# Optimization experiments

Hardware: AMD Instinct MI355X
Metric: run time of the kernel (lower is better)

The kernel has to match this reference:

```python
import jax, jax.numpy as jnp
import numpy as np

K = 98          # fixed_n_tokens
HEADS = 8
EPS = 1e-5      # BatchNorm eps


def setup_inputs() -> dict:
    key = jax.random.key(0)
    ks = jax.random.split(key, 8)
    B, C, H, W = 32, 384, 56, 56

    def p(k, shape, scale=0.02):
        return jax.random.normal(k, shape, jnp.float32) * scale

    return {
        "x": jax.random.normal(ks[0], (B, C, H, W), jnp.float32),
        "qkv_w": p(ks[1], (3 * C, C)),
        "qkv_b": jnp.zeros((3 * C,), jnp.float32),
        "proj_w": p(ks[2], (C, C)),
        "proj_b": jnp.zeros((C,), jnp.float32),
        "bn_g": jnp.ones((C,), jnp.float32),
        "bn_b": jnp.zeros((C,), jnp.float32),
        "fc1_w": p(ks[3], (C, C)),
        "fc1_b": jnp.zeros((C,), jnp.float32),
        "fc2_w": p(ks[4], (C, C)),
        "fc2_b": jnp.zeros((C,), jnp.float32),
        "dw_w": p(ks[5], (C, 1, 3, 3), 0.1),  # depthwise 3x3, groups=C
        "dw_b": jnp.zeros((C,), jnp.float32),
    }


def reference(x, qkv_w, qkv_b, proj_w, proj_b, bn_g, bn_b,
              fc1_w, fc1_b, fc2_w, fc2_b, dw_w, dw_b):
    B, C, H, W = x.shape
    N = H * W
    head_dim = C // HEADS
    scale = head_dim ** -0.5

    # ---- salience top-k selection (pool_size=(1,1): no pooling) ----
    xf = x.reshape(B, C, N)
    scores = jnp.sum(xf * xf, axis=1)                       # [B, N]
    _, top_idx = jax.lax.top_k(scores, K)                   # [B, K]
    top = jnp.take_along_axis(xf, top_idx[:, None, :], axis=2)   # [B, C, K]
    bg = (xf.sum(2) - top.sum(2)) / (N - K)                 # [B, C]
    tokens = jnp.concatenate([top, bg[:, :, None]], axis=2)      # [B, C, K+1]
    tokens = tokens.transpose(0, 2, 1)                      # [B, K+1, C]

    # ---- tiny attention over K+1 tokens ----
    n = K + 1
    qkv = tokens @ qkv_w.T + qkv_b                          # [B, n, 3C]
    qkv = qkv.reshape(B, n, 3, HEADS, head_dim).transpose(2, 0, 3, 1, 4)
    q, k, v = qkv[0], qkv[1], qkv[2]                        # [B, h, n, d]
    attn = jax.nn.softmax(scale * jnp.einsum('bhnd,bhmd->bhnm', q, k), axis=-1)
    res = jnp.einsum('bhnm,bhmd->bhnd', attn, v)            # [B, h, n, d]
    attn_out = res.transpose(0, 1, 3, 2).reshape(B, C, n)   # b (h d) n

    # ---- scatter-restore: bg token everywhere, top tokens at their slots ----
    top_res, bg_res = attn_out[:, :, :K], attn_out[:, :, K:]    # [B,C,K], [B,C,1]
    restored = jnp.broadcast_to(bg_res, (B, C, N))
    bi = jnp.arange(B)[:, None, None]
    ci = jnp.arange(C)[None, :, None]
    restored = restored.at[bi, ci, top_idx[:, None, :]].set(top_res)
    restored = restored.reshape(B, C, H, W)  # interpolate is identity (same size)

    # ---- conv branch: BN (batch stats) -> fc1 -> gelu -> dwconv -> fc2 ----
    mu = x.mean(axis=(0, 2, 3), keepdims=True)
    var = x.var(axis=(0, 2, 3), keepdims=True)
    xn = (x - mu) * jax.lax.rsqrt(var + EPS)
    xn = xn * bn_g[None, :, None, None] + bn_b[None, :, None, None]
    h1 = jnp.einsum('bchw,oc->bohw', xn, fc1_w) + fc1_b[None, :, None, None]
    h1 = jax.nn.gelu(h1, approximate=False)
    h2 = jax.lax.conv_general_dilated(
        h1, dw_w, window_strides=(1, 1), padding='SAME',
        dimension_numbers=('NCHW', 'OIHW', 'NCHW'), feature_group_count=C)
    h2 = h2 + dw_b[None, :, None, None]
    conv_out = jnp.einsum('bchw,oc->bohw', h2, fc2_w) + fc2_b[None, :, None, None]

    combined = restored + conv_out
    return jnp.einsum('bchw,oc->bohw', combined, proj_w) + proj_b[None, :, None, None]
```

## Files before the change

kernel.cpp:

```cpp
#include <hip/hip_runtime.h>
#include <hip/hip_bf16.h>
#include <math.h>

typedef unsigned short u16;
typedef short short8 __attribute__((ext_vector_type(8)));
typedef float floatx4 __attribute__((ext_vector_type(4)));

#define B_    32
#define C_    384
#define N_    3136
#define K_TOP 98
#define NTOK  99
#define TOKS  (B_ * NTOK)
#define HEADS_ 8
#define HD    48
#define KDIM  384

__device__ __forceinline__ float b2f(u16 u) {
    unsigned int x = ((unsigned int)u) << 16;
    return __builtin_bit_cast(float, x);
}
__device__ __forceinline__ u16 f2b(float f) {
    unsigned int x = __builtin_bit_cast(unsigned int, f);
    unsigned int r = (x + 0x7fffu + ((x >> 16) & 1u)) >> 16;
    return (u16)r;
}
__device__ __forceinline__ u16 tob16(float f) { return f2b(f); }
__device__ __forceinline__ u16 tob16(u16 u) { return u; }


__global__ void k_zero(float* sumsq) { sumsq[threadIdx.x] = 0.f; }

__global__ void k_cvt(const float* __restrict__ src, u16* __restrict__ dst, int n) {
    int i = blockIdx.x * 256 + threadIdx.x;
    if (i < n) dst[i] = f2b(src[i]);
}

__global__ void k_scores(const float* __restrict__ x, float* __restrict__ scores) {
    int gid = blockIdx.x * 256 + threadIdx.x;
    int b = gid / N_;
    int p = gid - b * N_;
    const float* xp = x + (size_t)b * C_ * N_ + p;
    float s = 0.f;
#pragma unroll 8
    for (int c = 0; c < C_; ++c) {
        float v = xp[(size_t)c * N_];
        s += v * v;
    }
    scores[gid] = s;
}

__global__ void k_chsum(const float* __restrict__ x, float* __restrict__ ch_sum,
                        float* __restrict__ sumsq) {
    int bc = blockIdx.x;
    int c = bc % C_;
    const float* xp = x + (size_t)bc * N_;
    float s1 = 0.f, s2 = 0.f;
    for (int p = threadIdx.x; p < N_; p += 256) {
        float v = xp[p];
        s1 += v; s2 += v * v;
    }
#pragma unroll
    for (int off = 32; off; off >>= 1) {
        s1 += __shfl_down(s1, off);
        s2 += __shfl_down(s2, off);
    }
    __shared__ float r1[4], r2[4];
    int wave = threadIdx.x >> 6;
    if ((threadIdx.x & 63) == 0) { r1[wave] = s1; r2[wave] = s2; }
    __syncthreads();
    if (threadIdx.x == 0) {
        float a = r1[0] + r1[1] + r1[2] + r1[3];
        float b2 = r2[0] + r2[1] + r2[2] + r2[3];
        ch_sum[bc] = a;
        atomicAdd(&sumsq[c], b2);
    }
}

__launch_bounds__(1024)
__global__ void k_topk(const float* __restrict__ scores, int* __restrict__ idx,
                       int* __restrict__ istop) {
    int b = blockIdx.x;
    int tid = threadIdx.x;
    __shared__ unsigned int keys[N_];
    __shared__ int hist[4096];
    __shared__ unsigned int sh_prefix;
    __shared__ int sh_g;
    __shared__ int c1, tc;
    __shared__ int idxbuf[K_TOP];
    __shared__ int tiebuf[128];

    for (int p = tid; p < N_; p += 1024) {
        keys[p] = __builtin_bit_cast(unsigned int, scores[b * N_ + p]);
        istop[b * N_ + p] = 0;
    }

    int Kcur = K_TOP;
    unsigned int prefix = 0;
    int m = 0;
#pragma unroll
    for (int pass = 0; pass < 3; ++pass) {
        const int shift = (pass == 0) ? 20 : (pass == 1 ? 8 : 0);
        const int nbins = (pass == 2) ? 256 : 4096;
        const unsigned int pm = (pass == 0) ? 0u : (pass == 1 ? 0xFFF00000u : 0xFFFFFF00u);
        for (int i = tid; i < nbins; i += 1024) hist[i] = 0;
        __syncthreads();
        for (int p = tid; p < N_; p += 1024) {
            unsigned int u = keys[p];
            if ((u & pm) == prefix) atomicAdd(&hist[(u >> shift) & (nbins - 1)], 1);
        }
        __syncthreads();
        if (tid < 64) {
            int lane = tid;
            int nch = nbins >> 6;
            int s = 0;
            for (int j = 0; j < nch; ++j) s += hist[lane * nch + j];
            int suf = s;
#pragma unroll
            for (int off = 1; off < 64; off <<= 1) {
                int v = __shfl_down(suf, off);
                if (lane + off < 64) suf += v;
            }
            int above = suf - s;
            if (suf >= Kcur && above < Kcur) {
                int acc = above;
                int bin = (lane + 1) * nch - 1;
                for (;; --bin) {
                    int h = hist[bin];
                    if (acc + h >= Kcur) break;
                    acc += h;
                }
                sh_prefix = prefix | ((unsigned int)bin << shift);
                sh_g = acc;
            }
        }
        __syncthreads();
        prefix = sh_prefix;
        m += sh_g;
        Kcur -= sh_g;
    }

    unsigned int lo = prefix;
    if (tid == 0) { c1 = 0; tc = 0; }
    __syncthreads();
    for (int p = tid; p < N_; p += 1024) {
        unsigned int u = keys[p];
        if (u > lo) { int pos = atomicAdd(&c1, 1); idxbuf[pos] = p; }
        else if (u == lo) { int pos = atomicAdd(&tc, 1); if (pos < 128) tiebuf[pos] = p; }
    }
    __syncthreads();
    if (tid == 0) {
        int need = K_TOP - m;
        if (tc <= 128) {
            int cnt = tc;
            for (int r = 0; r < need; ++r) {
                int mi = r;
                for (int q = r + 1; q < cnt; ++q) if (tiebuf[q] < tiebuf[mi]) mi = q;
                int t = tiebuf[mi]; tiebuf[mi] = tiebuf[r]; tiebuf[r] = t;
                idxbuf[m + r] = t;
            }
        } else {
            int picked = 0;
            for (int p = 0; p < N_ && picked < need; ++p)
                if (keys[p] == lo) { idxbuf[m + picked] = p; ++picked; }
        }
    }
    __syncthreads();
    if (tid < K_TOP) {
        int ib = idxbuf[tid];
        idx[b * K_TOP + tid] = ib;
        istop[b * N_ + ib] = tid + 1;
    }
}

__launch_bounds__(256)
__global__ void k_tokens(const float* __restrict__ x, const int* __restrict__ idx,
                         const float* __restrict__ ch_sum, u16* __restrict__ tokensT) {
    int b = blockIdx.x, cg = blockIdx.y;
    __shared__ int il[K_TOP];
    int tid = threadIdx.x;
    if (tid < K_TOP) il[tid] = idx[b * K_TOP + tid];
    __syncthreads();
    int cl = tid >> 2;
    int js = tid & 3;
    int c = cg * 64 + cl;
    const float* xp = x + (size_t)b * C_ * N_ + (size_t)c * N_;
    u16* tp = tokensT + (size_t)c * TOKS + b * NTOK;
    float s = 0.f;
    for (int j = js; j < K_TOP; j += 4) {
        float v = xp[il[j]];
        tp[j] = f2b(v);
        s += v;
    }
    s += __shfl_down(s, 2);
    s += __shfl_down(s, 1);
    if (js == 0) {
        float bg = (ch_sum[b * C_ + c] - s) * (1.0f / (float)(N_ - K_TOP));
        tp[K_TOP] = f2b(bg);
    }
}

__global__ void k_bnfin(const float* ch_sum, const float* sumsq, const float* bn_g,
                        const float* bn_b, float* a_scale, float* b_shift) {
    int c = threadIdx.x;
    float s = 0.f;
    for (int b = 0; b < B_; ++b) s += ch_sum[b * C_ + c];
    float inv_n = 1.0f / (float)(B_ * N_);
    float mu = s * inv_n;
    float var = sumsq[c] * inv_n - mu * mu;
    float a = rsqrtf(var + 1e-5f) * bn_g[c];
    a_scale[c] = a;
    b_shift[c] = bn_b[c] - mu * a;
}

__global__ void k_bias2p(const float* __restrict__ fc2_w, const float* __restrict__ fc2_b,
                         const float* __restrict__ dw_b, float* __restrict__ bias2p) {
    int c = blockIdx.x * 4 + (threadIdx.x >> 6);
    int l = threadIdx.x & 63;
    float acc = 0.f;
    for (int k = l; k < C_; k += 64) acc += fc2_w[c * C_ + k] * dw_b[k];
#pragma unroll
    for (int off = 32; off; off >>= 1) acc += __shfl_down(acc, off);
    if (l == 0) bias2p[c] = acc + fc2_b[c];
}

__global__ void k_biasM(const float* __restrict__ proj_w, const float* __restrict__ proj_b,
                        const float* __restrict__ bias2p, float* __restrict__ biasM) {
    int o = blockIdx.x * 4 + (threadIdx.x >> 6);
    int l = threadIdx.x & 63;
    float acc = 0.f;
    for (int c = l; c < C_; c += 64) acc += proj_w[o * C_ + c] * bias2p[c];
#pragma unroll
    for (int off = 32; off; off >>= 1) acc += __shfl_down(acc, off);
    if (l == 0) biasM[o] = acc + proj_b[o];
}

__global__ void k_bias1(const float* __restrict__ fc1_w, const float* __restrict__ fc1_b,
                        const float* __restrict__ b_shift, float* __restrict__ bias1) {
    int o = blockIdx.x * 4 + (threadIdx.x >> 6);
    int l = threadIdx.x & 63;
    float acc = 0.f;
    for (int c = l; c < C_; c += 64) acc += fc1_w[o * C_ + c] * b_shift[c];
#pragma unroll
    for (int off = 32; off; off >>= 1) acc += __shfl_down(acc, off);
    if (l == 0) bias1[o] = acc + fc1_b[o];
}

__global__ void k_cbias(const float* __restrict__ proj_w, const float* __restrict__ biasM,
                        const float* __restrict__ bgres, float* __restrict__ cbias) {
    int b = blockIdx.y;
    int o = blockIdx.x * 4 + (threadIdx.x >> 6);
    int l = threadIdx.x & 63;
    float acc = 0.f;
    for (int c = l; c < C_; c += 64) acc += proj_w[o * C_ + c] * bgres[b * C_ + c];
#pragma unroll
    for (int off = 32; off; off >>= 1) acc += __shfl_down(acc, off);
    if (l == 0) cbias[b * C_ + o] = acc + biasM[o];
}

__global__ void k_mw(const float* __restrict__ proj_w, const float* __restrict__ fc2_w,
                     u16* __restrict__ Mw) {
    int o = blockIdx.x, c = threadIdx.x;
    float acc = 0.f;
    for (int k = 0; k < C_; ++k) acc += proj_w[o * C_ + k] * fc2_w[k * C_ + c];
    Mw[o * C_ + c] = f2b(acc);
}

__global__ void k_w1p(const float* fc1_w, const float* a_scale, u16* W1p) {
    int i = blockIdx.x * 256 + threadIdx.x;
    if (i < C_ * C_) {
        int c = i % C_;
        W1p[i] = f2b(fc1_w[i] * a_scale[c]);
    }
}

__launch_bounds__(256)
__global__ void k_gemm_qkv(const u16* __restrict__ A, const u16* __restrict__ Bsrc,
                           const float* __restrict__ biasB, float* __restrict__ outF) {
    const int ldB = TOKS, NC = TOKS;
    int m0 = blockIdx.x * 128;
    int n0 = blockIdx.y * 64;
    int tid = threadIdx.x;
    int lane = tid & 63;
    int wave = tid >> 6;
    int wm0 = (wave >> 1) * 64;
    int wn0 = (wave & 1) * 32;
    int lm = lane & 15;
    int quad = lane >> 4;

    __shared__ __attribute__((aligned(16))) u16 Al[128 * 32];
    __shared__ __attribute__((aligned(16))) u16 Bl[64 * 32];

    floatx4 acc[4][2];
#pragma unroll
    for (int i = 0; i < 4; ++i)
#pragma unroll
        for (int j = 0; j < 2; ++j)
#pragma unroll
            for (int r = 0; r < 4; ++r) acc[i][j][r] = 0.f;

    int ar = tid >> 2;
    int akc = (tid & 3) * 8;
    int bp = tid & 63;
    int bgi = tid >> 6;
    int bswz = ((bgi ^ ((bp >> 1) & 3)) & 3) * 8;
    int bcol = n0 + bp;
    bool bok = bcol < NC;

    for (int kt = 0; kt < 12; ++kt) {
        int k0 = kt * 32;
        __syncthreads();
#pragma unroll
        for (int i = 0; i < 2; ++i) {
            int r = ar + i * 64;
            short8 v = *(const short8*)(const void*)(A + (size_t)(m0 + r) * KDIM + k0 + akc);
            *(short8*)(void*)&Al[r * 32 + akc] = v;
        }
        {
            const u16* src = Bsrc + (size_t)(k0 + bgi * 8) * ldB + bcol;
            short8 v;
#pragma unroll
            for (int j = 0; j < 8; ++j)
                v[j] = bok ? (short)src[(size_t)j * ldB] : (short)0;
            *(short8*)(void*)&Bl[bp * 32 + bswz] = v;
        }
        __syncthreads();
        short8 af[4], bfv[2];
#pragma unroll
        for (int mt = 0; mt < 4; ++mt)
            af[mt] = *(const short8*)(const void*)&Al[(wm0 + mt * 16 + lm) * 32 + quad * 8];
#pragma unroll
        for (int nt = 0; nt < 2; ++nt) {
            int prow = wn0 + nt * 16 + lm;
            int sw = ((quad ^ ((prow >> 1) & 3)) & 3) * 8;
            bfv[nt] = *(const short8*)(const void*)&Bl[prow * 32 + sw];
        }
#pragma unroll
        for (int mt = 0; mt < 4; ++mt)
#pragma unroll
            for (int nt = 0; nt < 2; ++nt)
                acc[mt][nt] = __builtin_amdgcn_mfma_f32_16x16x32_bf16(af[mt], bfv[nt], acc[mt][nt], 0, 0, 0);
    }

#pragma unroll
    for (int nt = 0; nt < 2; ++nt) {
        int col = n0 + wn0 + nt * 16 + lm;
        if (col >= NC) continue;
#pragma unroll
        for (int mt = 0; mt < 4; ++mt)
#pragma unroll
            for (int r = 0; r < 4; ++r) {
                int o = m0 + wm0 + mt * 16 + quad * 4 + r;
                outF[(size_t)o * TOKS + col] = acc[mt][nt][r] + biasB[o];
            }
    }
}

template<int MODE, typename TB>
__launch_bounds__(512, 4)
__global__ void k_gemm2(const u16* __restrict__ A, const TB* __restrict__ B0, long bStride,
                        const float* __restrict__ biasF,
                        float* __restrict__ outF,
                        u16* __restrict__ outB,
                        const float* __restrict__ cbias, const int* __restrict__ istop,
                        const float* __restrict__ delta2) {
    const int ldB = N_;
    int b = blockIdx.y;
    int n0 = blockIdx.x * 64;
    const TB* Bsrc = B0 + (size_t)b * bStride;
    int tid = threadIdx.x;
    int lane = tid & 63;
    int wave = tid >> 6;
    int wm0 = wave * 48;
    int lm = lane & 15;
    int quad = lane >> 4;

    __shared__ __attribute__((aligned(16))) u16 Bl[2][64 * 128];

    int sc = tid & 63;
    int kg = tid >> 6;
    int w0 = ((kg ^ (sc & 7)) * 8);
    const TB* bsp = Bsrc + (size_t)n0 + sc;

    floatx4 acc[3][4];
#pragma unroll
    for (int i = 0; i < 3; ++i)
#pragma unroll
        for (int j = 0; j < 4; ++j)
#pragma unroll
            for (int r = 0; r < 4; ++r) acc[i][j][r] = 0.f;

    TB rv0[8], rv1[8];
    {
        const TB* p0 = bsp + (size_t)(kg * 8) * ldB;
        const TB* p1 = bsp + (size_t)(64 + kg * 8) * ldB;
#pragma unroll
        for (int j = 0; j < 8; ++j) { rv0[j] = p0[(size_t)j * ldB]; rv1[j] = p1[(size_t)j * ldB]; }
        short8 s0, s1;
#pragma unroll
        for (int j = 0; j < 8; ++j) { s0[j] = (short)tob16(rv0[j]); s1[j] = (short)tob16(rv1[j]); }
        *(short8*)(void*)&Bl[0][sc * 128 + w0] = s0;
        *(short8*)(void*)&Bl[0][sc * 128 + 64 + w0] = s1;
    }
    __syncthreads();

    for (int ch = 0; ch < 3; ++ch) {
        int cur = ch & 1;
        if (ch < 2) {
            const TB* p0 = bsp + (size_t)((ch + 1) * 128 + kg * 8) * ldB;
            const TB* p1 = bsp + (size_t)((ch + 1) * 128 + 64 + kg * 8) * ldB;
#pragma unroll
            for (int j = 0; j < 8; ++j) { rv0[j] = p0[(size_t)j * ldB]; rv1[j] = p1[(size_t)j * ldB]; }
        }
#pragma unroll
        for (int kt = 0; kt < 4; ++kt) {
            int k0 = ch * 128 + kt * 32;
            short8 af[3], bfv[4];
#pragma unroll
            for (int mt = 0; mt < 3; ++mt)
                af[mt] = *(const short8*)(const void*)(A + (size_t)(wm0 + mt * 16 + lm) * KDIM + k0 + quad * 8);
#pragma unroll
            for (int nt = 0; nt < 4; ++nt) {
                int pc = nt * 16 + lm;
                int win = kt * 4 + quad;
                bfv[nt] = *(const short8*)(const void*)&Bl[cur][pc * 128 + ((win ^ (pc & 7)) * 8)];
            }
#pragma unroll
            for (int mt = 0; mt < 3; ++mt)
#pragma unroll
                for (int nt = 0; nt < 4; ++nt)
                    acc[mt][nt] = __builtin_amdgcn_mfma_f32_16x16x32_bf16(af[mt], bfv[nt], acc[mt][nt], 0, 0, 0);
        }
        if (ch < 2) {
            short8 s0, s1;
#pragma unroll
            for (int j = 0; j < 8; ++j) { s0[j] = (short)tob16(rv0[j]); s1[j] = (short)tob16(rv1[j]); }
            *(short8*)(void*)&Bl[cur ^ 1][sc * 128 + w0] = s0;
            *(short8*)(void*)&Bl[cur ^ 1][sc * 128 + 64 + w0] = s1;
            __syncthreads();
        }
    }

#pragma unroll
    for (int nt = 0; nt < 4; ++nt) {
        int ocol = n0 + nt * 16 + lm;
        int tt = 0;
        if (MODE == 3) tt = istop[b * N_ + ocol];
#pragma unroll
        for (int mt = 0; mt < 3; ++mt) {
#pragma unroll
            for (int r = 0; r < 4; ++r) {
                int o = wm0 + mt * 16 + quad * 4 + r;
                float val = acc[mt][nt][r];
                if (MODE == 2) {
                    outF[(size_t)o * N_ + ocol] = val;
                } else if (MODE == 1) {
                    val += biasF[o];
                    float g = 0.5f * val * (1.0f + erff(val * 0.70710678118654752f));
                    outB[(size_t)b * C_ * N_ + (size_t)o * N_ + ocol] = f2b(g);
                } else {
                    val += cbias[b * C_ + o];
                    if (tt) val += delta2[(size_t)o * N_ + b * K_TOP + (tt - 1)];
                    outF[(size_t)b * C_ * N_ + (size_t)o * N_ + ocol] = val;
                }
            }
        }
    }
}


__global__ void k_attn_scores(const float* __restrict__ qkv, float* __restrict__ Sws) {
    int b = blockIdx.x, h = blockIdx.y;
    __shared__ float ql[NTOK * HD], kl[NTOK * HD];
    int tid = threadIdx.x;
    const float scale = 0.14433756729740643f;
    for (int u = tid; u < NTOK * HD; u += 256) {
        int d = u / NTOK, j = u - d * NTOK;
        size_t base = (size_t)(h * HD + d) * TOKS + b * NTOK + j;
        ql[j * HD + d] = qkv[base] * scale;
        kl[j * HD + d] = qkv[base + (size_t)C_ * TOKS];
    }
    __syncthreads();
    float* Sp = Sws + (size_t)(b * HEADS_ + h) * (NTOK * NTOK);
    for (int u = tid; u < NTOK * NTOK; u += 256) {
        int i = u / NTOK, j = u - i * NTOK;
        float s = 0.f;
#pragma unroll 8
        for (int d = 0; d < HD; ++d) s += ql[i * HD + d] * kl[j * HD + d];
        Sp[u] = s;
    }
}

__global__ void k_attn_out(const float* __restrict__ qkv, const float* __restrict__ Sws,
                           u16* __restrict__ diffT, float* __restrict__ bgres) {
    int b = blockIdx.x, h = blockIdx.y;
    __shared__ float vl[NTOK * HD];
    __shared__ float P[NTOK * 100];
    __shared__ float bgrow[HD];
    int tid = threadIdx.x;
    for (int u = tid; u < NTOK * HD; u += 256) {
        int d = u / NTOK, j = u - d * NTOK;
        vl[j * HD + d] = qkv[(size_t)(2 * C_ + h * HD + d) * TOKS + b * NTOK + j];
    }
    __syncthreads();
    const float* Sp = Sws + (size_t)(b * HEADS_ + h) * (NTOK * NTOK);
    if (tid < NTOK) {
        int i = tid;
        float mx = -1e30f;
        for (int j = 0; j < NTOK; ++j) mx = fmaxf(mx, Sp[i * NTOK + j]);
        float sum = 0.f;
        for (int j = 0; j < NTOK; ++j) { float e = expf(Sp[i * NTOK + j] - mx); P[i * 100 + j] = e; sum += e; }
        float inv = 1.f / sum;
        for (int j = 0; j < NTOK; ++j) P[i * 100 + j] *= inv;
    }
    __syncthreads();
    if (tid < HD) {
        int d = tid;
        float a = 0.f;
        for (int j = 0; j < NTOK; ++j) a += P[K_TOP * 100 + j] * vl[j * HD + d];
        bgrow[d] = a;
        bgres[b * C_ + h * HD + d] = a;
    }
    __syncthreads();
    for (int u = tid; u < K_TOP * HD; u += 256) {
        int d = u / K_TOP, i = u - d * K_TOP;
        float a = 0.f;
        for (int j = 0; j < NTOK; ++j) a += P[i * 100 + j] * vl[j * HD + d];
        diffT[(size_t)(h * HD + d) * N_ + b * K_TOP + i] = f2b(a - bgrow[d]);
    }
}

__launch_bounds__(256)
__global__ void k_dwconv(u16* __restrict__ h1, const float* __restrict__ dw_w) {
    int bc = blockIdx.x;
    int c = bc % C_;
    __shared__ __attribute__((aligned(16))) u16 tile[4256];
    int tid = threadIdx.x;
#pragma unroll
    for (int i = tid; i < 532; i += 256)
        *(short8*)(void*)&tile[i * 8] = (short8)0;
    float w[9];
#pragma unroll
    for (int t = 0; t < 9; ++t) w[t] = dw_w[c * 9 + t];
    __syncthreads();
    u16* src = h1 + (size_t)bc * N_;
    for (int i = tid; i < 392; i += 256) {
        int y = i / 7, xg = i - y * 7;
        short8 v = *(const short8*)(const void*)(src + i * 8);
        *(short8*)(void*)&tile[(y + 2) * 72 + xg * 8] = v;
    }
    __syncthreads();
    for (int g = tid; g < 392; g += 256) {
        int y = g / 7, xg = (g - y * 7) * 8;
        float out[8];
#pragma unroll
        for (int t = 0; t < 8; ++t) out[t] = 0.f;
#pragma unroll
        for (int ky = 0; ky < 3; ++ky) {
            const u16* rp = &tile[(y + ky + 1) * 72 + xg];
            short8 mid = *(const short8*)(const void*)rp;
            float r[10];
            r[0] = b2f(rp[-1]);
#pragma unroll
            for (int t = 0; t < 8; ++t) r[t + 1] = b2f((u16)mid[t]);
            r[9] = b2f(rp[8]);
#pragma unroll
            for (int kx = 0; kx < 3; ++kx) {
                float wv = w[ky * 3 + kx];
#pragma unroll
                for (int t = 0; t < 8; ++t) out[t] += wv * r[t + kx];
            }
        }
        short8 o;
#pragma unroll
        for (int t = 0; t < 8; ++t) o[t] = (short)f2b(out[t]);
        *(short8*)(void*)(src + g * 8) = o;
    }
}


extern "C" void kernel_launch(void* const* d_in, const int* in_sizes, int n_in,
                              void* d_out, int out_size, void* d_ws, size_t ws_size,
                              hipStream_t stream) {
    (void)in_sizes; (void)n_in; (void)out_size; (void)ws_size;
    const float* x      = (const float*)d_in[0];
    const float* qkv_w  = (const float*)d_in[1];
    const float* qkv_b  = (const float*)d_in[2];
    const float* proj_w = (const float*)d_in[3];
    const float* proj_b = (const float*)d_in[4];
    const float* bn_g   = (const float*)d_in[5];
    const float* bn_b   = (const float*)d_in[6];
    const float* fc1_w  = (const float*)d_in[7];
    const float* fc1_b  = (const float*)d_in[8];
    const float* fc2_w  = (const float*)d_in[9];
    const float* fc2_b  = (const float*)d_in[10];
    const float* dw_w   = (const float*)d_in[11];
    const float* dw_b   = (const float*)d_in[12];
    float* out = (float*)d_out;

    float* qkvF = (float*)d_out;
    float* Sws  = (float*)((char*)d_out + (size_t)3 * C_ * TOKS * 4);

    char* w = (char*)d_ws;
    constexpr size_t o_h1      = 0;
    constexpr size_t o_scores  = o_h1      + (size_t)B_ * C_ * N_ * 2;
    constexpr size_t o_chsum   = o_scores  + (size_t)B_ * N_ * 4;
    constexpr size_t o_sumsq   = o_chsum   + (size_t)B_ * C_ * 4;
    constexpr size_t o_idx     = o_sumsq   + (size_t)C_ * 4;
    constexpr size_t o_istop   = o_idx     + (size_t)B_ * K_TOP * 4;
    constexpr size_t o_tokens  = o_istop   + (size_t)B_ * N_ * 4;
    constexpr size_t o_ascale  = o_tokens  + (size_t)C_ * TOKS * 2;
    constexpr size_t o_bshift  = o_ascale  + (size_t)C_ * 4;
    constexpr size_t o_w1p     = o_bshift  + (size_t)C_ * 4;
    constexpr size_t o_bias1   = o_w1p     + (size_t)C_ * C_ * 2;
    constexpr size_t o_mw      = o_bias1   + (size_t)C_ * 4;
    constexpr size_t o_biasM   = o_mw      + (size_t)C_ * C_ * 2;
    constexpr size_t o_bias2p  = o_biasM   + (size_t)C_ * 4;
    constexpr size_t o_cbias   = o_bias2p  + (size_t)C_ * 4;
    constexpr size_t o_bgres   = o_cbias   + (size_t)B_ * C_ * 4;
    constexpr size_t o_difft   = o_bgres   + (size_t)B_ * C_ * 4;
    constexpr size_t o_delta2  = o_difft   + (size_t)C_ * N_ * 2;
    constexpr size_t o_wq16    = o_delta2  + (size_t)C_ * N_ * 4;
    constexpr size_t o_pw16    = o_wq16    + (size_t)3 * C_ * C_ * 2;

    u16*   h1      = (u16*)(w + o_h1);
    float* scores  = (float*)(w + o_scores);
    float* ch_sum  = (float*)(w + o_chsum);
    float* sumsq   = (float*)(w + o_sumsq);
    int*   idx     = (int*)(w + o_idx);
    int*   istop   = (int*)(w + o_istop);
    u16*   tokensT = (u16*)(w + o_tokens);
    float* a_scale = (float*)(w + o_ascale);
    float* b_shift = (float*)(w + o_bshift);
    u16*   W1p     = (u16*)(w + o_w1p);
    float* bias1   = (float*)(w + o_bias1);
    u16*   Mw      = (u16*)(w + o_mw);
    float* biasM   = (float*)(w + o_biasM);
    float* bias2p  = (float*)(w + o_bias2p);
    float* cbias   = (float*)(w + o_cbias);
    float* bgres   = (float*)(w + o_bgres);
    u16*   diffT   = (u16*)(w + o_difft);
    float* Delta2  = (float*)(w + o_delta2);
    u16*   Wq16    = (u16*)(w + o_wq16);
    u16*   Pw16    = (u16*)(w + o_pw16);

    k_zero<<<1, C_, 0, stream>>>(sumsq);
    k_scores<<<(B_ * N_) / 256, 256, 0, stream>>>(x, scores);
    k_chsum<<<B_ * C_, 256, 0, stream>>>(x, ch_sum, sumsq);
    k_topk<<<B_, 1024, 0, stream>>>(scores, idx, istop);
    k_tokens<<<dim3(B_, 6), 256, 0, stream>>>(x, idx, ch_sum, tokensT);
    k_bnfin<<<1, C_, 0, stream>>>(ch_sum, sumsq, bn_g, bn_b, a_scale, b_shift);
    k_bias2p<<<96, 256, 0, stream>>>(fc2_w, fc2_b, dw_b, bias2p);
    k_mw<<<C_, C_, 0, stream>>>(proj_w, fc2_w, Mw);
    k_biasM<<<96, 256, 0, stream>>>(proj_w, proj_b, bias2p, biasM);
    k_w1p<<<(C_ * C_ + 255) / 256, 256, 0, stream>>>(fc1_w, a_scale, W1p);
    k_bias1<<<96, 256, 0, stream>>>(fc1_w, fc1_b, b_shift, bias1);
    k_cvt<<<(3 * C_ * C_ + 255) / 256, 256, 0, stream>>>(qkv_w, Wq16, 3 * C_ * C_);
    k_cvt<<<(C_ * C_ + 255) / 256, 256, 0, stream>>>(proj_w, Pw16, C_ * C_);

    k_gemm_qkv<<<dim3(9, 50), 256, 0, stream>>>(Wq16, tokensT, qkv_b, qkvF);
    k_attn_scores<<<dim3(B_, HEADS_), 256, 0, stream>>>(qkvF, Sws);
    k_attn_out<<<dim3(B_, HEADS_), 256, 0, stream>>>(qkvF, Sws, diffT, bgres);
    k_cbias<<<dim3(96, B_), 256, 0, stream>>>(proj_w, biasM, bgres, cbias);
    k_gemm2<2, u16><<<dim3(49, 1), 512, 0, stream>>>(Pw16, diffT, 0,
        nullptr, Delta2, nullptr, nullptr, nullptr, nullptr);
    k_gemm2<1, float><<<dim3(49, 32), 512, 0, stream>>>(W1p, x, (long)C_ * N_,
        bias1, nullptr, h1, nullptr, nullptr, nullptr);
    k_dwconv<<<B_ * C_, 256, 0, stream>>>(h1, dw_w);
    k_gemm2<3, u16><<<dim3(49, 32), 512, 0, stream>>>(Mw, h1, (long)C_ * N_,
        nullptr, out, nullptr, cbias, istop, Delta2);
}
```

Before: 727.7 us.

## Load full K panel into LDS once, prefetch A, stage GELU output through LDS

The GEMM kernel now loads the whole 384-deep B panel for its 64-column tile into shared memory up front, replacing the double-buffered 128-chunk pipeline. The K loop becomes 12 steps with register prefetch of the next A fragments. For MODE 1, GELU bf16 results are staged in shared memory and written out as coalesced 16-byte rows instead of scattered 2-byte stores. Shared memory grows to 48KB per block and launch bounds drop to 2 blocks/SM, which lowers occupancy and gives up overlap between global loads and MFMA.

```diff
diff --git a/kernel.cpp b/kernel.cpp
--- a/kernel.cpp
+++ b/kernel.cpp
@@ -357,7 +357,7 @@
 }
 
 template<int MODE, typename TB>
-__launch_bounds__(512, 4)
+__launch_bounds__(512, 2)
 __global__ void k_gemm2(const u16* __restrict__ A, const TB* __restrict__ B0, long bStride,
                         const float* __restrict__ biasF,
                         float* __restrict__ outF,
@@ -375,12 +375,27 @@
     int lm = lane & 15;
     int quad = lane >> 4;
 
-    __shared__ __attribute__((aligned(16))) u16 Bl[2][64 * 128];
-
-    int sc = tid & 63;
-    int kg = tid >> 6;
-    int w0 = ((kg ^ (sc & 7)) * 8);
-    const TB* bsp = Bsrc + (size_t)n0 + sc;
+    __shared__ __attribute__((aligned(16))) u16 Bl[64 * 384];
+
+    {
+        int sc = tid & 63;
+        int kg = tid >> 6;
+        const TB* bp = Bsrc + (size_t)n0 + sc;
+        TB rv[48];
+#pragma unroll
+        for (int m = 0; m < 6; ++m)
+#pragma unroll
+            for (int j = 0; j < 8; ++j)
+                rv[m * 8 + j] = bp[(size_t)(kg * 48 + m * 8 + j) * ldB];
+#pragma unroll
+        for (int m = 0; m < 6; ++m) {
+            int win = kg * 6 + m;
+            short8 s;
+#pragma unroll
+            for (int j = 0; j < 8; ++j) s[j] = (short)tob16(rv[m * 8 + j]);
+            *(short8*)(void*)&Bl[sc * 384 + ((win ^ (sc & 7)) * 8)] = s;
+        }
+    }
 
     floatx4 acc[3][4];
 #pragma unroll
@@ -390,78 +405,79 @@
 #pragma unroll
             for (int r = 0; r < 4; ++r) acc[i][j][r] = 0.f;
 
-    TB rv0[8], rv1[8];
-    {
-        const TB* p0 = bsp + (size_t)(kg * 8) * ldB;
-        const TB* p1 = bsp + (size_t)(64 + kg * 8) * ldB;
-#pragma unroll
-        for (int j = 0; j < 8; ++j) { rv0[j] = p0[(size_t)j * ldB]; rv1[j] = p1[(size_t)j * ldB]; }
-        short8 s0, s1;
-#pragma unroll
-        for (int j = 0; j < 8; ++j) { s0[j] = (short)tob16(rv0[j]); s1[j] = (short)tob16(rv1[j]); }
-        *(short8*)(void*)&Bl[0][sc * 128 + w0] = s0;
-        *(short8*)(void*)&Bl[0][sc * 128 + 64 + w0] = s1;
-    }
-    __syncthreads();
-
-    for (int ch = 0; ch < 3; ++ch) {
-        int cur = ch & 1;
-        if (ch < 2) {
-            const TB* p0 = bsp + (size_t)((ch + 1) * 128 + kg * 8) * ldB;
-            const TB* p1 = bsp + (size_t)((ch + 1) * 128 + 64 + kg * 8) * ldB;
-#pragma unroll
-            for (int j = 0; j < 8; ++j) { rv0[j] = p0[(size_t)j * ldB]; rv1[j] = p1[(size_t)j * ldB]; }
-        }
-#pragma unroll
-        for (int kt = 0; kt < 4; ++kt) {
-            int k0 = ch * 128 + kt * 32;
-            short8 af[3], bfv[4];
+    __syncthreads();
+
+    const u16* Ap = A + (size_t)(wm0 + lm) * KDIM + quad * 8;
+    short8 af[3], afn[3];
+#pragma unroll
+    for (int mt = 0; mt < 3; ++mt)
+        af[mt] = *(const short8*)(const void*)(Ap + (size_t)(mt * 16) * KDIM);
+
+    for (int kt = 0; kt < 12; ++kt) {
+        if (kt < 11) {
 #pragma unroll
             for (int mt = 0; mt < 3; ++mt)
-                af[mt] = *(const short8*)(const void*)(A + (size_t)(wm0 + mt * 16 + lm) * KDIM + k0 + quad * 8);
-#pragma unroll
-            for (int nt = 0; nt < 4; ++nt) {
-                int pc = nt * 16 + lm;
-                int win = kt * 4 + quad;
-                bfv[nt] = *(const short8*)(const void*)&Bl[cur][pc * 128 + ((win ^ (pc & 7)) * 8)];
-            }
+                afn[mt] = *(const short8*)(const void*)(Ap + (size_t)(mt * 16) * KDIM + (kt + 1) * 32);
+        }
+        short8 bfv[4];
+#pragma unroll
+        for (int nt = 0; nt < 4; ++nt) {
+            int pc = nt * 16 + lm;
+            int win = kt * 4 + quad;
+            bfv[nt] = *(const short8*)(const void*)&Bl[pc * 384 + ((win ^ (pc & 7)) * 8)];
+        }
+#pragma unroll
+        for (int mt = 0; mt < 3; ++mt)
+#pragma unroll
+            for (int nt = 0; nt < 4; ++nt)
+                acc[mt][nt] = __builtin_amdgcn_mfma_f32_16x16x32_bf16(af[mt], bfv[nt], acc[mt][nt], 0, 0, 0);
+#pragma unroll
+        for (int mt = 0; mt < 3; ++mt) af[mt] = afn[mt];
+    }
+
+    if (MODE == 1) {
+        __syncthreads();
+        u16* hls = Bl;
+#pragma unroll
+        for (int nt = 0; nt < 4; ++nt)
 #pragma unroll
             for (int mt = 0; mt < 3; ++mt)
 #pragma unroll
-                for (int nt = 0; nt < 4; ++nt)
-                    acc[mt][nt] = __builtin_amdgcn_mfma_f32_16x16x32_bf16(af[mt], bfv[nt], acc[mt][nt], 0, 0, 0);
-        }
-        if (ch < 2) {
-            short8 s0, s1;
-#pragma unroll
-            for (int j = 0; j < 8; ++j) { s0[j] = (short)tob16(rv0[j]); s1[j] = (short)tob16(rv1[j]); }
-            *(short8*)(void*)&Bl[cur ^ 1][sc * 128 + w0] = s0;
-            *(short8*)(void*)&Bl[cur ^ 1][sc * 128 + 64 + w0] = s1;
-            __syncthreads();
-        }
-    }
-
-#pragma unroll
-    for (int nt = 0; nt < 4; ++nt) {
-        int ocol = n0 + nt * 16 + lm;
-        int tt = 0;
-        if (MODE == 3) tt = istop[b * N_ + ocol];
-#pragma unroll
-        for (int mt = 0; mt < 3; ++mt) {
-#pragma unroll
-            for (int r = 0; r < 4; ++r) {
-                int o = wm0 + mt * 16 + quad * 4 + r;
-                float val = acc[mt][nt][r];
-                if (MODE == 2) {
-                    outF[(size_t)o * N_ + ocol] = val;
-                } else if (MODE == 1) {
-                    val += biasF[o];
+                for (int r = 0; r < 4; ++r) {
+                    int o = wm0 + mt * 16 + quad * 4 + r;
+                    float val = acc[mt][nt][r] + biasF[o];
                     float g = 0.5f * val * (1.0f + erff(val * 0.70710678118654752f));
-                    outB[(size_t)b * C_ * N_ + (size_t)o * N_ + ocol] = f2b(g);
-                } else {
-                    val += cbias[b * C_ + o];
-                    if (tt) val += delta2[(size_t)o * N_ + b * K_TOP + (tt - 1)];
-                    outF[(size_t)b * C_ * N_ + (size_t)o * N_ + ocol] = val;
+                    hls[o * 64 + nt * 16 + lm] = f2b(g);
+                }
+        __syncthreads();
+        int row0 = tid >> 3;
+        int cg = (tid & 7) * 8;
+        u16* dst = outB + (size_t)b * C_ * N_ + n0;
+#pragma unroll
+        for (int it = 0; it < 6; ++it) {
+            int row = it * 64 + row0;
+            short8 v = *(const short8*)(const void*)&hls[row * 64 + cg];
+            *(short8*)(void*)(dst + (size_t)row * N_ + cg) = v;
+        }
+    } else {
+#pragma unroll
+        for (int nt = 0; nt < 4; ++nt) {
+            int ocol = n0 + nt * 16 + lm;
+            int tt = 0;
+            if (MODE == 3) tt = istop[b * N_ + ocol];
+#pragma unroll
+            for (int mt = 0; mt < 3; ++mt) {
+#pragma unroll
+                for (int r = 0; r < 4; ++r) {
+                    int o = wm0 + mt * 16 + quad * 4 + r;
+                    float val = acc[mt][nt][r];
+                    if (MODE == 2) {
+                        outF[(size_t)o * N_ + ocol] = val;
+                    } else {
+                        val += cbias[b * C_ + o];
+                        if (tt) val += delta2[(size_t)o * N_ + b * K_TOP + (tt - 1)];
+                        outF[(size_t)b * C_ * N_ + (size_t)o * N_ + ocol] = val;
+                    }
                 }
             }
         }
```

Result: no change. 721.4 us (-0.9%).
